# Kernel optimization log

Measured on AMD Instinct MI355X. Metric: run time of the kernel, lower is better.

Reference implementation:

```python
import jax, jax.numpy as jnp
import numpy as np

B, S, NX, NH = 4, 1024, 1024, 16
HD = NX // NH  # head_features = 64


def setup_inputs() -> dict:
    key = jax.random.key(0)
    k1, k2, k3 = jax.random.split(key, 3)
    x = jax.random.normal(k1, (B, S, NX), dtype=jnp.float32)
    w_attn = 0.02 * jax.random.normal(k2, (NX, 3 * NX), dtype=jnp.float32)
    b_attn = jnp.zeros((3 * NX,), dtype=jnp.float32)
    w_proj = 0.02 * jax.random.normal(k3, (NX, NX), dtype=jnp.float32)
    b_proj = jnp.zeros((NX,), dtype=jnp.float32)
    causal_bias = jnp.tril(jnp.ones((S, S), dtype=jnp.float32))  # tril buffer
    return {"x": x, "w_attn": w_attn, "b_attn": b_attn,
            "w_proj": w_proj, "b_proj": b_proj, "causal_bias": causal_bias}


def reference(x, w_attn, b_attn, w_proj, b_proj, causal_bias):
    # c_attn: fused qkv projection (Conv1D == addmm)
    qkv = x @ w_attn + b_attn                     # [B, S, 3*NX]
    q, k, v = jnp.split(qkv, 3, axis=-1)          # each [B, S, NX]
    # split heads -> [B, H, S, D]
    q = q.reshape(B, S, NH, HD).transpose(0, 2, 1, 3)
    k = k.reshape(B, S, NH, HD).transpose(0, 2, 1, 3)
    v = v.reshape(B, S, NH, HD).transpose(0, 2, 1, 3)
    # present: stack of (key in [B,H,S,D] layout, value)
    present = jnp.stack((k, v))                   # [2, B, H, S, D]
    # scores with scale=True
    w = jnp.einsum('bhqd,bhkd->bhqk', q, k) / jnp.sqrt(jnp.float32(HD))
    b = causal_bias[None, None, :, :]             # [1,1,S,S] (nd==ns==S)
    w = w * b - 1e10 * (1.0 - b)                  # multiplicative mask trick
    p = jax.nn.softmax(w, axis=-1)
    a = jnp.einsum('bhqk,bhkd->bhqd', p, v)       # [B, H, S, D]
    a = a.transpose(0, 2, 1, 3).reshape(B, S, NX)  # merge heads
    out = a @ w_proj + b_proj                     # c_proj
    return out, present
```

## Files before the change

kernel.cpp:

```cpp
#include <hip/hip_runtime.h>
#include <hip/hip_bf16.h>

typedef __attribute__((ext_vector_type(8))) short short8;
typedef __attribute__((ext_vector_type(4))) float floatx4;

constexpr int Bsz = 4, Ssz = 1024, NXc = 1024, NHc = 16, HDc = 64;
constexpr int OUT_ELEMS  = Bsz * Ssz * NXc;
constexpr int HEAD_ELEMS = Bsz * NHc * Ssz * HDc;

union BF8 { __hip_bfloat16 h[8]; uint4 v; short8 s; };

__device__ __forceinline__ uint4 cvt8(const float* __restrict__ p) {
    float4 a = *reinterpret_cast<const float4*>(p);
    float4 b = *reinterpret_cast<const float4*>(p + 4);
    BF8 u;
    u.h[0] = __float2bfloat16(a.x); u.h[1] = __float2bfloat16(a.y);
    u.h[2] = __float2bfloat16(a.z); u.h[3] = __float2bfloat16(a.w);
    u.h[4] = __float2bfloat16(b.x); u.h[5] = __float2bfloat16(b.y);
    u.h[6] = __float2bfloat16(b.z); u.h[7] = __float2bfloat16(b.w);
    return u.v;
}

__device__ __forceinline__ void load_lds_16B(const void* g, void* l) {
    __builtin_amdgcn_global_load_lds(
        (const __attribute__((address_space(1))) unsigned int*)g,
        (__attribute__((address_space(3))) unsigned int*)l, 16, 0, 0);
}


__global__ __launch_bounds__(256) void prep_kernel(
    const float* __restrict__ x, __hip_bfloat16* __restrict__ x_bf,
    const float* __restrict__ w_attn, __hip_bfloat16* __restrict__ wTa,
    const float* __restrict__ w_proj, __hip_bfloat16* __restrict__ wTp)
{
    const int bid = blockIdx.x, tid = threadIdx.x;
    __shared__ float t[64][65];
    if (bid < 2048) {
        const int i = (bid * 256 + tid) * 8;
        *reinterpret_cast<uint4*>(x_bf + i) = cvt8(x + i);
        return;
    }
    const float* in; __hip_bfloat16* outp; int N, bx, by;
    if (bid < 2816) { const int q = bid - 2048; in = w_attn; outp = wTa; N = 3072; bx = q % 48; by = q / 48; }
    else            { const int q = bid - 2816; in = w_proj; outp = wTp; N = 1024; bx = q % 16; by = q / 16; }
    const int k0 = by * 64, n0 = bx * 64;
#pragma unroll
    for (int j = 0; j < 16; ++j) {
        const int idx = tid + j * 256;
        const int row = idx >> 6, col = idx & 63;
        t[row][col] = in[(size_t)(k0 + row) * N + n0 + col];
    }
    __syncthreads();
#pragma unroll
    for (int j = 0; j < 16; ++j) {
        const int idx = tid + j * 256;
        const int orow = idx >> 6, ocol = idx & 63;
        outp[(size_t)(n0 + orow) * 1024 + k0 + ocol] = __float2bfloat16(t[ocol][orow]);
    }
}

template <int EPI>
__global__ __launch_bounds__(256) void gemm128p(
    const __hip_bfloat16* __restrict__ A,
    const __hip_bfloat16* __restrict__ Bt,
    const float* __restrict__ bias,
    float* __restrict__ outf,
    __hip_bfloat16* __restrict__ qws,
    float* __restrict__ present,
    __hip_bfloat16* __restrict__ kws,
    __hip_bfloat16* __restrict__ vtws,
    int M, int N, int K)
{
    __shared__ __align__(16) __hip_bfloat16 As[3][4096];
    __shared__ __align__(16) __hip_bfloat16 Bs[3][4096];

    const int nbx = N >> 7;
    const int nwg = (M >> 7) * nbx;
    const int wg  = blockIdx.x;
    const int swz = (wg & 7) * (nwg >> 3) + (wg >> 3);
    const int by  = swz / nbx, bx = swz % nbx;

    const int tid  = threadIdx.x;
    const int w    = tid >> 6, lane = tid & 63;
    const int quad = lane >> 4, l16 = lane & 15;
    const int m0 = by * 128, n0 = bx * 128;
    const int mb = (w >> 1) * 64, nbw = (w & 1) * 64;

    const int srow = lane >> 2;
    const int sksw = (((lane & 3) ^ ((lane >> 3) & 3))) * 8;
    const int rsw = (l16 >> 1) & 3;

    floatx4 acc[4][4];
#pragma unroll
    for (int i = 0; i < 4; ++i)
#pragma unroll
        for (int j = 0; j < 4; ++j)
#pragma unroll
            for (int r = 0; r < 4; ++r) acc[i][j][r] = 0.f;

    auto stage = [&](int buf, int k0) {
#pragma unroll
        for (int c = 0; c < 2; ++c) {
            const int chunk = w * 2 + c;
            const int row = chunk * 16 + srow;
            load_lds_16B(A + (size_t)(m0 + row) * K + k0 + sksw,
                         &As[buf][chunk * 512]);
            load_lds_16B(Bt + (size_t)(n0 + row) * K + k0 + sksw,
                         &Bs[buf][chunk * 512]);
        }
    };

    stage(0, 0);
    int cb = 0;
    for (int k0 = 0; k0 < K; k0 += 32) {
        if (k0 + 32 < K) {
            const int nb_ = (cb == 2) ? 0 : cb + 1;
            stage(nb_, k0 + 32);
            asm volatile("s_waitcnt vmcnt(4)" ::: "memory");
        } else {
            asm volatile("s_waitcnt vmcnt(0)" ::: "memory");
        }
        __builtin_amdgcn_s_barrier();
        __builtin_amdgcn_sched_barrier(0);

        short8 af[4], bfr[4];
#pragma unroll
        for (int mi = 0; mi < 4; ++mi)
            af[mi] = *reinterpret_cast<const short8*>(
                &As[cb][(mb + mi * 16 + l16) * 32 + ((quad ^ rsw) * 8)]);
#pragma unroll
        for (int ni = 0; ni < 4; ++ni)
            bfr[ni] = *reinterpret_cast<const short8*>(
                &Bs[cb][(nbw + ni * 16 + l16) * 32 + ((quad ^ rsw) * 8)]);
        __builtin_amdgcn_s_setprio(1);
#pragma unroll
        for (int mi = 0; mi < 4; ++mi)
#pragma unroll
            for (int ni = 0; ni < 4; ++ni)
                acc[mi][ni] = __builtin_amdgcn_mfma_f32_16x16x32_bf16(
                    af[mi], bfr[ni], acc[mi][ni], 0, 0, 0);
        __builtin_amdgcn_s_setprio(0);

        cb = (cb == 2) ? 0 : cb + 1;
    }

#pragma unroll
    for (int mi = 0; mi < 4; ++mi) {
#pragma unroll
        for (int ni = 0; ni < 4; ++ni) {
            const int col = n0 + nbw + ni * 16 + l16;
            const float bsv = bias[col];
#pragma unroll
            for (int r = 0; r < 4; ++r) {
                const int row = m0 + mb + mi * 16 + quad * 4 + r;
                const float v = acc[mi][ni][r] + bsv;
                if (EPI == 0) {
                    const int seg = col >> 10;
                    const int c = col & 1023;
                    if (seg == 0) {
                        qws[(size_t)row * 1024 + c] = __float2bfloat16(v);
                    } else {
                        const int bq = row >> 10, s = row & 1023;
                        const int hh = c >> 6, d = c & 63;
                        const size_t idx =
                            ((size_t)((bq * 16 + hh) * 1024 + s)) * 64 + d;
                        const int kt = s >> 6, key = s & 63;
                        const size_t tbase =
                            ((size_t)((bq * 16 + hh) * 16 + kt)) * 4096;
                        if (seg == 1) {
                            present[idx] = v;
                            kws[tbase + key * 64 +
                                ((((d >> 3) ^ (key & 7)) << 3) | (d & 7))] =
                                __float2bfloat16(v);
                        } else {
                            present[HEAD_ELEMS + idx] = v;
                            vtws[tbase + d * 64 +
                                ((((key >> 3) ^ (d & 7)) << 3) | (key & 7))] =
                                __float2bfloat16(v);
                        }
                    }
                } else {
                    outf[(size_t)row * N + col] = v;
                }
            }
        }
    }
}

__global__ __launch_bounds__(256) void attn_v5(
    const __hip_bfloat16* __restrict__ q_ws,
    const __hip_bfloat16* __restrict__ k_ws,
    const __hip_bfloat16* __restrict__ vt_ws,
    __hip_bfloat16* __restrict__ a_ws)
{
    const int wg  = blockIdx.x;
    const int swz = (wg & 7) * 128 + (wg >> 3);
    const int qt  = 15 - (swz & 15);
    const int bh  = swz >> 4;
    const int b = bh >> 4, h = bh & 15;

    const int tid  = threadIdx.x;
    const int wave = tid >> 6, lane = tid & 63;
    const int quad = lane >> 4, l16 = lane & 15;
    const int stripe = wave * 16;

    const __hip_bfloat16* Kbase = k_ws  + (size_t)bh * 65536;
    const __hip_bfloat16* Vbase = vt_ws + (size_t)bh * 65536;

    __shared__ __align__(16) __hip_bfloat16 Ksf[2][4096];
    __shared__ __align__(16) __hip_bfloat16 Vsf[2][4096];
    __shared__ __align__(16) __hip_bfloat16 Ps[64][72];

    constexpr float SCL = 0.18033688011f;

    const __hip_bfloat16* Qb =
        q_ws + ((size_t)(b * Ssz + qt * 64 + stripe + l16)) * NXc + h * 64;
    const short8 qf0 = *reinterpret_cast<const short8*>(Qb + quad * 8);
    const short8 qf1 = *reinterpret_cast<const short8*>(Qb + 32 + quad * 8);

    float m_i[4], l_i[4];
#pragma unroll
    for (int r = 0; r < 4; ++r) { m_i[r] = -1e9f; l_i[r] = 0.f; }
    floatx4 oacc[4];
#pragma unroll
    for (int ni = 0; ni < 4; ++ni)
#pragma unroll
        for (int r = 0; r < 4; ++r) oacc[ni][r] = 0.f;

#pragma unroll
    for (int c2 = 0; c2 < 2; ++c2) {
        const int c = wave + c2 * 4;
        load_lds_16B(Kbase + c * 512 + (lane << 3), &Ksf[0][c * 512]);
        load_lds_16B(Vbase + c * 512 + (lane << 3), &Vsf[0][c * 512]);
    }

    int cw = 0;
    for (int kt = 0; kt <= qt; ++kt) {
        asm volatile("s_waitcnt vmcnt(0)" ::: "memory");
        __builtin_amdgcn_s_barrier();
        __builtin_amdgcn_sched_barrier(0);

        if (kt < qt) {
            const __hip_bfloat16* Kt = Kbase + (size_t)(kt + 1) * 4096;
            const __hip_bfloat16* Vt = Vbase + (size_t)(kt + 1) * 4096;
            const int nb_ = cw ^ 1;
#pragma unroll
            for (int c2 = 0; c2 < 2; ++c2) {
                const int c = wave + c2 * 4;
                load_lds_16B(Kt + c * 512 + (lane << 3), &Ksf[nb_][c * 512]);
                load_lds_16B(Vt + c * 512 + (lane << 3), &Vsf[nb_][c * 512]);
            }
        }

        floatx4 sacc[4];
#pragma unroll
        for (int ni = 0; ni < 4; ++ni)
#pragma unroll
            for (int r = 0; r < 4; ++r) sacc[ni][r] = 0.f;
        __builtin_amdgcn_s_setprio(1);
#pragma unroll
        for (int ni = 0; ni < 4; ++ni) {
            const int key = ni * 16 + l16;
            const int sw = key & 7;
            const short8 kf0 = *reinterpret_cast<const short8*>(
                &Ksf[cw][key * 64 + ((quad ^ sw) << 3)]);
            const short8 kf1 = *reinterpret_cast<const short8*>(
                &Ksf[cw][key * 64 + (((4 + quad) ^ sw) << 3)]);
            sacc[ni] = __builtin_amdgcn_mfma_f32_16x16x32_bf16(
                qf0, kf0, sacc[ni], 0, 0, 0);
            sacc[ni] = __builtin_amdgcn_mfma_f32_16x16x32_bf16(
                qf1, kf1, sacc[ni], 0, 0, 0);
        }
        __builtin_amdgcn_s_setprio(0);

        const bool diag = (kt == qt);
        float alpha_[4];
#pragma unroll
        for (int r = 0; r < 4; ++r) {
            const int lrow = stripe + quad * 4 + r;
            float sv[4];
            float mx = -1e30f;
#pragma unroll
            for (int ni = 0; ni < 4; ++ni) {
                float v = sacc[ni][r] * SCL;
                if (diag && (ni * 16 + l16) > lrow) v = -1e9f;
                sv[ni] = v;
                mx = fmaxf(mx, v);
            }
            mx = fmaxf(mx, __shfl_xor(mx, 1));
            mx = fmaxf(mx, __shfl_xor(mx, 2));
            mx = fmaxf(mx, __shfl_xor(mx, 4));
            mx = fmaxf(mx, __shfl_xor(mx, 8));
            const float mnew = fmaxf(m_i[r], mx);
            const float al = exp2f(m_i[r] - mnew);
            m_i[r] = mnew;
            float s = 0.f;
#pragma unroll
            for (int nn = 0; nn < 4; ++nn) {
                const int ni = (nn + quad) & 3;
                const float p = exp2f(sv[ni] - mnew);
                s += p;
                Ps[lrow][ni * 16 + l16] = __float2bfloat16(p);
            }
            s += __shfl_xor(s, 1);
            s += __shfl_xor(s, 2);
            s += __shfl_xor(s, 4);
            s += __shfl_xor(s, 8);
            l_i[r] = l_i[r] * al + s;
            alpha_[r] = al;
        }

#pragma unroll
        for (int ni = 0; ni < 4; ++ni)
#pragma unroll
            for (int r = 0; r < 4; ++r) oacc[ni][r] *= alpha_[r];

        __builtin_amdgcn_s_setprio(1);
#pragma unroll
        for (int kk = 0; kk < 64; kk += 32) {
            const short8 pf = *reinterpret_cast<const short8*>(
                &Ps[stripe + l16][kk + quad * 8]);
#pragma unroll
            for (int ni = 0; ni < 4; ++ni) {
                const int d = ni * 16 + l16;
                const int chunk = (kk >> 3) + quad;
                const short8 vf = *reinterpret_cast<const short8*>(
                    &Vsf[cw][d * 64 + ((chunk ^ (d & 7)) << 3)]);
                oacc[ni] = __builtin_amdgcn_mfma_f32_16x16x32_bf16(
                    pf, vf, oacc[ni], 0, 0, 0);
            }
        }
        __builtin_amdgcn_s_setprio(0);

        cw ^= 1;
    }

#pragma unroll
    for (int ni = 0; ni < 4; ++ni) {
#pragma unroll
        for (int r = 0; r < 4; ++r) {
            const int row = qt * 64 + stripe + quad * 4 + r;
            const int col = h * 64 + ni * 16 + l16;
            const float inv = 1.0f / fmaxf(l_i[r], 1e-20f);
            a_ws[((size_t)(b * Ssz + row)) * NXc + col] =
                __float2bfloat16(oacc[ni][r] * inv);
        }
    }
}

template <int EPI>
__global__ __launch_bounds__(256) void gemm64(
    const void* __restrict__ Av, const float* __restrict__ Bw,
    const float* __restrict__ bias, float* __restrict__ out0,
    float* __restrict__ present, int M, int N, int K)
{
    __shared__ __align__(16) __hip_bfloat16 As[64][40];
    __shared__ __align__(16) __hip_bfloat16 Bs[64][40];
    const int tid = threadIdx.x;
    const int wave = tid >> 6, lane = tid & 63;
    const int quad = lane >> 4, l16 = lane & 15;
    const int m0 = blockIdx.y * 64, n0 = blockIdx.x * 64;
    const int mb = (wave >> 1) * 32, nb = (wave & 1) * 32;
    const int arow = tid >> 2, aseg = tid & 3;
    const int brow = tid >> 3, bseg = tid & 7;
    floatx4 acc[2][2];
#pragma unroll
    for (int i = 0; i < 2; ++i)
#pragma unroll
        for (int j = 0; j < 2; ++j)
#pragma unroll
            for (int r = 0; r < 4; ++r) acc[i][j][r] = 0.f;
    for (int k0 = 0; k0 < K; k0 += 32) {
        if (EPI == 0) {
            const float* A = (const float*)Av;
            *reinterpret_cast<uint4*>(&As[arow][aseg * 8]) =
                cvt8(A + (size_t)(m0 + arow) * K + k0 + aseg * 8);
        } else {
            const __hip_bfloat16* A = (const __hip_bfloat16*)Av;
            *reinterpret_cast<uint4*>(&As[arow][aseg * 8]) =
                *reinterpret_cast<const uint4*>(
                    A + (size_t)(m0 + arow) * K + k0 + aseg * 8);
        }
        const float* bp = Bw + (size_t)(k0 + brow) * N + n0 + bseg * 8;
        float4 b0 = *reinterpret_cast<const float4*>(bp);
        float4 b1 = *reinterpret_cast<const float4*>(bp + 4);
        Bs[bseg * 8 + 0][brow] = __float2bfloat16(b0.x);
        Bs[bseg * 8 + 1][brow] = __float2bfloat16(b0.y);
        Bs[bseg * 8 + 2][brow] = __float2bfloat16(b0.z);
        Bs[bseg * 8 + 3][brow] = __float2bfloat16(b0.w);
        Bs[bseg * 8 + 4][brow] = __float2bfloat16(b1.x);
        Bs[bseg * 8 + 5][brow] = __float2bfloat16(b1.y);
        Bs[bseg * 8 + 6][brow] = __float2bfloat16(b1.z);
        Bs[bseg * 8 + 7][brow] = __float2bfloat16(b1.w);
        __syncthreads();
        short8 af[2], bf[2];
#pragma unroll
        for (int mm = 0; mm < 2; ++mm)
            af[mm] = *reinterpret_cast<const short8*>(&As[mb + mm * 16 + l16][quad * 8]);
#pragma unroll
        for (int nn = 0; nn < 2; ++nn)
            bf[nn] = *reinterpret_cast<const short8*>(&Bs[nb + nn * 16 + l16][quad * 8]);
#pragma unroll
        for (int mm = 0; mm < 2; ++mm)
#pragma unroll
            for (int nn = 0; nn < 2; ++nn)
                acc[mm][nn] = __builtin_amdgcn_mfma_f32_16x16x32_bf16(
                    af[mm], bf[nn], acc[mm][nn], 0, 0, 0);
        __syncthreads();
    }
#pragma unroll
    for (int mm = 0; mm < 2; ++mm)
#pragma unroll
        for (int nn = 0; nn < 2; ++nn) {
            const int col = n0 + nb + nn * 16 + l16;
            const float bsv = bias[col];
#pragma unroll
            for (int r = 0; r < 4; ++r) {
                const int row = m0 + mb + mm * 16 + quad * 4 + r;
                const float v = acc[mm][nn][r] + bsv;
                if (EPI == 0) {
                    const int seg = col >> 10;
                    const int c = col & 1023;
                    if (seg == 0) out0[(size_t)row * 1024 + c] = v;
                    else {
                        const int b = row >> 10, s = row & 1023;
                        const int h = c >> 6, d = c & 63;
                        const size_t idx = ((size_t)((b * 16 + h) * 1024 + s)) * 64 + d;
                        if (seg == 1) present[idx] = v;
                        else          present[HEAD_ELEMS + idx] = v;
                    }
                } else out0[(size_t)row * N + col] = v;
            }
        }
}

__global__ __launch_bounds__(256) void attn64(
    const float* __restrict__ qbuf, const float* __restrict__ present,
    __hip_bfloat16* __restrict__ a_ws)
{
    const int qt = blockIdx.x, h = blockIdx.y, b = blockIdx.z;
    const int tid = threadIdx.x;
    const int wave = tid >> 6, lane = tid & 63;
    const int quad = lane >> 4, l16 = lane & 15;
    const int mb = (wave >> 1) * 32, nb = (wave & 1) * 32;
    const size_t headoff = ((size_t)(b * 16 + h)) * Ssz * HDc;
    const float* Qb = qbuf + ((size_t)(b * Ssz + qt * 64)) * NXc + h * 64;
    const float* Kp = present + headoff;
    const float* Vp = present + HEAD_ELEMS + headoff;
    __shared__ __align__(16) __hip_bfloat16 Qs[64][72];
    __shared__ __align__(16) __hip_bfloat16 Ks[64][72];
    __shared__ __align__(16) __hip_bfloat16 Vts[64][72];
    __shared__ __align__(16) __hip_bfloat16 Ps[64][72];
    __shared__ float Sc[64][65];
    __shared__ float mrow[64], lrow[64], arw[64];
#pragma unroll
    for (int it = 0; it < 2; ++it) {
        const int c = tid + it * 256;
        const int row = c >> 3, seg = c & 7;
        *reinterpret_cast<uint4*>(&Qs[row][seg * 8]) =
            cvt8(Qb + (size_t)row * NXc + seg * 8);
    }
    if (tid < 64) { mrow[tid] = -1e9f; lrow[tid] = 0.f; }
    floatx4 oacc[2][2];
#pragma unroll
    for (int i = 0; i < 2; ++i)
#pragma unroll
        for (int j = 0; j < 2; ++j)
#pragma unroll
            for (int r = 0; r < 4; ++r) oacc[i][j][r] = 0.f;
    __syncthreads();
    for (int kt = 0; kt <= qt; ++kt) {
#pragma unroll
        for (int it = 0; it < 2; ++it) {
            const int c = tid + it * 256;
            const int row = c >> 3, seg = c & 7;
            *reinterpret_cast<uint4*>(&Ks[row][seg * 8]) =
                cvt8(Kp + (size_t)(kt * 64 + row) * 64 + seg * 8);
            const float* vp = Vp + (size_t)(kt * 64 + row) * 64 + seg * 8;
            float4 v0 = *reinterpret_cast<const float4*>(vp);
            float4 v1 = *reinterpret_cast<const float4*>(vp + 4);
            Vts[seg * 8 + 0][row] = __float2bfloat16(v0.x);
            Vts[seg * 8 + 1][row] = __float2bfloat16(v0.y);
            Vts[seg * 8 + 2][row] = __float2bfloat16(v0.z);
            Vts[seg * 8 + 3][row] = __float2bfloat16(v0.w);
            Vts[seg * 8 + 4][row] = __float2bfloat16(v1.x);
            Vts[seg * 8 + 5][row] = __float2bfloat16(v1.y);
            Vts[seg * 8 + 6][row] = __float2bfloat16(v1.z);
            Vts[seg * 8 + 7][row] = __float2bfloat16(v1.w);
        }
        __syncthreads();
        floatx4 sacc[2][2];
#pragma unroll
        for (int i = 0; i < 2; ++i)
#pragma unroll
            for (int j = 0; j < 2; ++j)
#pragma unroll
                for (int r = 0; r < 4; ++r) sacc[i][j][r] = 0.f;
#pragma unroll
        for (int kd = 0; kd < 64; kd += 32) {
            short8 af[2], bf[2];
#pragma unroll
            for (int mm = 0; mm < 2; ++mm)
                af[mm] = *reinterpret_cast<const short8*>(&Qs[mb + mm * 16 + l16][kd + quad * 8]);
#pragma unroll
            for (int nn = 0; nn < 2; ++nn)
                bf[nn] = *reinterpret_cast<const short8*>(&Ks[nb + nn * 16 + l16][kd + quad * 8]);
#pragma unroll
            for (int mm = 0; mm < 2; ++mm)
#pragma unroll
                for (int nn = 0; nn < 2; ++nn)
                    sacc[mm][nn] = __builtin_amdgcn_mfma_f32_16x16x32_bf16(
                        af[mm], bf[nn], sacc[mm][nn], 0, 0, 0);
        }
        const bool diag = (kt == qt);
#pragma unroll
        for (int mm = 0; mm < 2; ++mm)
#pragma unroll
            for (int nn = 0; nn < 2; ++nn)
#pragma unroll
                for (int r = 0; r < 4; ++r) {
                    const int row = mb + mm * 16 + quad * 4 + r;
                    const int col = nb + nn * 16 + l16;
                    float v = fminf(fmaxf(sacc[mm][nn][r] * 0.125f, -1e8f), 1e8f);
                    if (diag && col > row) v = -1e9f;
                    Sc[row][col] = v;
                }
        __syncthreads();
        if (tid < 64) {
            const int r = tid;
            const float mo = mrow[r];
            float mx = mo;
            for (int c = 0; c < 64; ++c) mx = fmaxf(mx, Sc[r][c]);
            const float al = (mo <= -5e8f) ? 0.f : __expf(mo - mx);
            float sum = 0.f;
            for (int c = 0; c < 64; ++c) {
                const float sv = Sc[r][c];
                const float p = (sv <= -5e8f) ? 0.f : __expf(sv - mx);
                sum += p;
                Ps[r][c] = __float2bfloat16(p);
            }
            mrow[r] = mx;
            lrow[r] = lrow[r] * al + sum;
            arw[r]  = al;
        }
        __syncthreads();
#pragma unroll
        for (int mm = 0; mm < 2; ++mm) {
            const int rbase = mb + mm * 16 + quad * 4;
#pragma unroll
            for (int r = 0; r < 4; ++r) {
                const float al = arw[rbase + r];
                oacc[mm][0][r] *= al;
                oacc[mm][1][r] *= al;
            }
        }
#pragma unroll
        for (int kk = 0; kk < 64; kk += 32) {
            short8 pf[2], vf[2];
#pragma unroll
            for (int mm = 0; mm < 2; ++mm)
                pf[mm] = *reinterpret_cast<const short8*>(&Ps[mb + mm * 16 + l16][kk + quad * 8]);
#pragma unroll
            for (int nn = 0; nn < 2; ++nn)
                vf[nn] = *reinterpret_cast<const short8*>(&Vts[nb + nn * 16 + l16][kk + quad * 8]);
#pragma unroll
            for (int mm = 0; mm < 2; ++mm)
#pragma unroll
                for (int nn = 0; nn < 2; ++nn)
                    oacc[mm][nn] = __builtin_amdgcn_mfma_f32_16x16x32_bf16(
                        pf[mm], vf[nn], oacc[mm][nn], 0, 0, 0);
        }
        __syncthreads();
    }
#pragma unroll
    for (int mm = 0; mm < 2; ++mm)
#pragma unroll
        for (int nn = 0; nn < 2; ++nn)
#pragma unroll
            for (int r = 0; r < 4; ++r) {
                const int row = mb + mm * 16 + quad * 4 + r;
                const int col = nb + nn * 16 + l16;
                const float inv = 1.0f / fmaxf(lrow[row], 1e-20f);
                a_ws[((size_t)(b * Ssz + qt * 64 + row)) * NXc + h * 64 + col] =
                    __float2bfloat16(oacc[mm][nn][r] * inv);
            }
}

extern "C" void kernel_launch(void* const* d_in, const int* in_sizes, int n_in,
                              void* d_out, int out_size, void* d_ws, size_t ws_size,
                              hipStream_t stream) {
    const float* x      = (const float*)d_in[0];
    const float* w_attn = (const float*)d_in[1];
    const float* b_attn = (const float*)d_in[2];
    const float* w_proj = (const float*)d_in[3];
    const float* b_proj = (const float*)d_in[4];

    float* out     = (float*)d_out;
    float* present = out + OUT_ELEMS;

    const size_t NEED = 32u * 1024u * 1024u;
    if (ws_size >= NEED) {
        __hip_bfloat16* reg1 = (__hip_bfloat16*)d_ws;
        __hip_bfloat16* reg2 = reg1 + 4194304;
        __hip_bfloat16* reg3 = reg2 + 4194304;
        __hip_bfloat16* wTa  = reg3 + 4194304;
        __hip_bfloat16* wTp  = wTa + 3145728;
        __hip_bfloat16* kws  = (__hip_bfloat16*)out;
        __hip_bfloat16* vtws = kws + 4194304;

        prep_kernel<<<3072, 256, 0, stream>>>(x, reg1, w_attn, wTa, w_proj, wTp);

        gemm128p<0><<<768, 256, 0, stream>>>(
            reg1, wTa, b_attn, nullptr, reg2, present, kws, vtws,
            4096, 3072, 1024);

        attn_v5<<<1024, 256, 0, stream>>>(reg2, kws, vtws, reg2);

        gemm128p<1><<<256, 256, 0, stream>>>(
            reg2, wTp, b_proj, out, nullptr, nullptr, nullptr, nullptr,
            4096, 1024, 1024);
    } else {
        __hip_bfloat16* a_ws = (__hip_bfloat16*)d_ws;
        hipMemsetAsync(d_ws, 0, (size_t)OUT_ELEMS * sizeof(__hip_bfloat16), stream);
        gemm64<0><<<dim3(48, 64), 256, 0, stream>>>(x, w_attn, b_attn, out, present,
                                                    4096, 3072, 1024);
        attn64<<<dim3(16, 16, 4), 256, 0, stream>>>(out, present, a_ws);
        gemm64<1><<<dim3(16, 64), 256, 0, stream>>>(a_ws, w_proj, b_proj, out, nullptr,
                                                    4096, 1024, 1024);
    }
}
```

Before: 213.7 us.

## Pair causal query tiles per block and deepen K/V prefetch to four buffers

```diff
diff --git a/kernel.cpp b/kernel.cpp
--- a/kernel.cpp
+++ b/kernel.cpp
@@ -187,16 +187,16 @@
     }
 }
 
-__global__ __launch_bounds__(256) void attn_v5(
+__global__ __launch_bounds__(256) void attn_v6(
     const __hip_bfloat16* __restrict__ q_ws,
     const __hip_bfloat16* __restrict__ k_ws,
     const __hip_bfloat16* __restrict__ vt_ws,
     __hip_bfloat16* __restrict__ a_ws)
 {
     const int wg  = blockIdx.x;
-    const int swz = (wg & 7) * 128 + (wg >> 3);
-    const int qt  = 15 - (swz & 15);
-    const int bh  = swz >> 4;
+    const int swz = (wg & 7) * 64 + (wg >> 3);
+    const int bx  = swz & 7;
+    const int bh  = swz >> 3;
     const int b = bh >> 4, h = bh & 15;
 
     const int tid  = threadIdx.x;
@@ -207,143 +207,161 @@
     const __hip_bfloat16* Kbase = k_ws  + (size_t)bh * 65536;
     const __hip_bfloat16* Vbase = vt_ws + (size_t)bh * 65536;
 
-    __shared__ __align__(16) __hip_bfloat16 Ksf[2][4096];
-    __shared__ __align__(16) __hip_bfloat16 Vsf[2][4096];
+    __shared__ __align__(16) __hip_bfloat16 Ksf[4][4096];
+    __shared__ __align__(16) __hip_bfloat16 Vsf[4][4096];
     __shared__ __align__(16) __hip_bfloat16 Ps[64][72];
 
     constexpr float SCL = 0.18033688011f;
 
-    const __hip_bfloat16* Qb =
-        q_ws + ((size_t)(b * Ssz + qt * 64 + stripe + l16)) * NXc + h * 64;
-    const short8 qf0 = *reinterpret_cast<const short8*>(Qb + quad * 8);
-    const short8 qf1 = *reinterpret_cast<const short8*>(Qb + 32 + quad * 8);
-
-    float m_i[4], l_i[4];
-#pragma unroll
-    for (int r = 0; r < 4; ++r) { m_i[r] = -1e9f; l_i[r] = 0.f; }
-    floatx4 oacc[4];
-#pragma unroll
-    for (int ni = 0; ni < 4; ++ni)
-#pragma unroll
-        for (int r = 0; r < 4; ++r) oacc[ni][r] = 0.f;
-
-#pragma unroll
-    for (int c2 = 0; c2 < 2; ++c2) {
-        const int c = wave + c2 * 4;
-        load_lds_16B(Kbase + c * 512 + (lane << 3), &Ksf[0][c * 512]);
-        load_lds_16B(Vbase + c * 512 + (lane << 3), &Vsf[0][c * 512]);
-    }
-
-    int cw = 0;
-    for (int kt = 0; kt <= qt; ++kt) {
-        asm volatile("s_waitcnt vmcnt(0)" ::: "memory");
-        __builtin_amdgcn_s_barrier();
-        __builtin_amdgcn_sched_barrier(0);
-
-        if (kt < qt) {
-            const __hip_bfloat16* Kt = Kbase + (size_t)(kt + 1) * 4096;
-            const __hip_bfloat16* Vt = Vbase + (size_t)(kt + 1) * 4096;
-            const int nb_ = cw ^ 1;
+#pragma unroll
+    for (int pass = 0; pass < 2; ++pass) {
+        const int qt = (pass == 0) ? (8 + bx) : (7 - bx);
+
+        const __hip_bfloat16* Qb =
+            q_ws + ((size_t)(b * Ssz + qt * 64 + stripe + l16)) * NXc + h * 64;
+        const short8 qf0 = *reinterpret_cast<const short8*>(Qb + quad * 8);
+        const short8 qf1 = *reinterpret_cast<const short8*>(Qb + 32 + quad * 8);
+
+        float m_i[4], l_i[4];
+#pragma unroll
+        for (int r = 0; r < 4; ++r) { m_i[r] = -1e9f; l_i[r] = 0.f; }
+        floatx4 oacc[4];
+#pragma unroll
+        for (int ni = 0; ni < 4; ++ni)
+#pragma unroll
+            for (int r = 0; r < 4; ++r) oacc[ni][r] = 0.f;
+
+#pragma unroll
+        for (int c2 = 0; c2 < 2; ++c2) {
+            const int c = wave + c2 * 4;
+            load_lds_16B(Kbase + c * 512 + (lane << 3), &Ksf[0][c * 512]);
+            load_lds_16B(Vbase + c * 512 + (lane << 3), &Vsf[0][c * 512]);
+        }
+        if (qt >= 1) {
 #pragma unroll
             for (int c2 = 0; c2 < 2; ++c2) {
                 const int c = wave + c2 * 4;
-                load_lds_16B(Kt + c * 512 + (lane << 3), &Ksf[nb_][c * 512]);
-                load_lds_16B(Vt + c * 512 + (lane << 3), &Vsf[nb_][c * 512]);
-            }
-        }
-
-        floatx4 sacc[4];
-#pragma unroll
-        for (int ni = 0; ni < 4; ++ni)
-#pragma unroll
-            for (int r = 0; r < 4; ++r) sacc[ni][r] = 0.f;
-        __builtin_amdgcn_s_setprio(1);
+                load_lds_16B(Kbase + 4096 + c * 512 + (lane << 3),
+                             &Ksf[1][c * 512]);
+                load_lds_16B(Vbase + 4096 + c * 512 + (lane << 3),
+                             &Vsf[1][c * 512]);
+            }
+        }
+
+        for (int kt = 0; kt <= qt; ++kt) {
+            const int cw = kt & 3;
+            if (kt + 2 <= qt) {
+                const int nb_ = (kt + 2) & 3;
+                const __hip_bfloat16* Kt = Kbase + (size_t)(kt + 2) * 4096;
+                const __hip_bfloat16* Vt = Vbase + (size_t)(kt + 2) * 4096;
+#pragma unroll
+                for (int c2 = 0; c2 < 2; ++c2) {
+                    const int c = wave + c2 * 4;
+                    load_lds_16B(Kt + c * 512 + (lane << 3), &Ksf[nb_][c * 512]);
+                    load_lds_16B(Vt + c * 512 + (lane << 3), &Vsf[nb_][c * 512]);
+                }
+                asm volatile("s_waitcnt vmcnt(8)" ::: "memory");
+            } else if (kt + 1 <= qt) {
+                asm volatile("s_waitcnt vmcnt(4)" ::: "memory");
+            } else {
+                asm volatile("s_waitcnt vmcnt(0)" ::: "memory");
+            }
+            __builtin_amdgcn_s_barrier();
+            __builtin_amdgcn_sched_barrier(0);
+
+            floatx4 sacc[4];
+#pragma unroll
+            for (int ni = 0; ni < 4; ++ni)
+#pragma unroll
+                for (int r = 0; r < 4; ++r) sacc[ni][r] = 0.f;
+            __builtin_amdgcn_s_setprio(1);
+#pragma unroll
+            for (int ni = 0; ni < 4; ++ni) {
+                const int key = ni * 16 + l16;
+                const int sw = key & 7;
+                const short8 kf0 = *reinterpret_cast<const short8*>(
+                    &Ksf[cw][key * 64 + ((quad ^ sw) << 3)]);
+                const short8 kf1 = *reinterpret_cast<const short8*>(
+                    &Ksf[cw][key * 64 + (((4 + quad) ^ sw) << 3)]);
+                sacc[ni] = __builtin_amdgcn_mfma_f32_16x16x32_bf16(
+                    qf0, kf0, sacc[ni], 0, 0, 0);
+                sacc[ni] = __builtin_amdgcn_mfma_f32_16x16x32_bf16(
+                    qf1, kf1, sacc[ni], 0, 0, 0);
+            }
+            __builtin_amdgcn_s_setprio(0);
+
+            const bool diag = (kt == qt);
+            float alpha_[4];
+#pragma unroll
+            for (int r = 0; r < 4; ++r) {
+                const int lrow = stripe + quad * 4 + r;
+                float sv[4];
+                float mx = -1e30f;
+#pragma unroll
+                for (int ni = 0; ni < 4; ++ni) {
+                    float v = sacc[ni][r] * SCL;
+                    if (diag && (ni * 16 + l16) > lrow) v = -1e9f;
+                    sv[ni] = v;
+                    mx = fmaxf(mx, v);
+                }
+                mx = fmaxf(mx, __shfl_xor(mx, 1));
+                mx = fmaxf(mx, __shfl_xor(mx, 2));
+                mx = fmaxf(mx, __shfl_xor(mx, 4));
+                mx = fmaxf(mx, __shfl_xor(mx, 8));
+                const float mnew = fmaxf(m_i[r], mx);
+                const float al = exp2f(m_i[r] - mnew);
+                m_i[r] = mnew;
+                float s = 0.f;
+#pragma unroll
+                for (int nn = 0; nn < 4; ++nn) {
+                    const int ni = (nn + quad) & 3;
+                    const float p = exp2f(sv[ni] - mnew);
+                    s += p;
+                    Ps[lrow][ni * 16 + l16] = __float2bfloat16(p);
+                }
+                s += __shfl_xor(s, 1);
+                s += __shfl_xor(s, 2);
+                s += __shfl_xor(s, 4);
+                s += __shfl_xor(s, 8);
+                l_i[r] = l_i[r] * al + s;
+                alpha_[r] = al;
+            }
+
+#pragma unroll
+            for (int ni = 0; ni < 4; ++ni)
+#pragma unroll
+                for (int r = 0; r < 4; ++r) oacc[ni][r] *= alpha_[r];
+
+            __builtin_amdgcn_s_setprio(1);
+#pragma unroll
+            for (int kk = 0; kk < 64; kk += 32) {
+                const short8 pf = *reinterpret_cast<const short8*>(
+                    &Ps[stripe + l16][kk + quad * 8]);
+#pragma unroll
+                for (int ni = 0; ni < 4; ++ni) {
+                    const int d = ni * 16 + l16;
+                    const int chunk = (kk >> 3) + quad;
+                    const short8 vf = *reinterpret_cast<const short8*>(
+                        &Vsf[cw][d * 64 + ((chunk ^ (d & 7)) << 3)]);
+                    oacc[ni] = __builtin_amdgcn_mfma_f32_16x16x32_bf16(
+                        pf, vf, oacc[ni], 0, 0, 0);
+                }
+            }
+            __builtin_amdgcn_s_setprio(0);
+        }
+
+        __builtin_amdgcn_s_barrier();
+
 #pragma unroll
         for (int ni = 0; ni < 4; ++ni) {
-            const int key = ni * 16 + l16;
-            const int sw = key & 7;
-            const short8 kf0 = *reinterpret_cast<const short8*>(
-                &Ksf[cw][key * 64 + ((quad ^ sw) << 3)]);
-            const short8 kf1 = *reinterpret_cast<const short8*>(
-                &Ksf[cw][key * 64 + (((4 + quad) ^ sw) << 3)]);
-            sacc[ni] = __builtin_amdgcn_mfma_f32_16x16x32_bf16(
-                qf0, kf0, sacc[ni], 0, 0, 0);
-            sacc[ni] = __builtin_amdgcn_mfma_f32_16x16x32_bf16(
-                qf1, kf1, sacc[ni], 0, 0, 0);
-        }
-        __builtin_amdgcn_s_setprio(0);
-
-        const bool diag = (kt == qt);
-        float alpha_[4];
-#pragma unroll
-        for (int r = 0; r < 4; ++r) {
-            const int lrow = stripe + quad * 4 + r;
-            float sv[4];
-            float mx = -1e30f;
-#pragma unroll
-            for (int ni = 0; ni < 4; ++ni) {
-                float v = sacc[ni][r] * SCL;
-                if (diag && (ni * 16 + l16) > lrow) v = -1e9f;
-                sv[ni] = v;
-                mx = fmaxf(mx, v);
-            }
-            mx = fmaxf(mx, __shfl_xor(mx, 1));
-            mx = fmaxf(mx, __shfl_xor(mx, 2));
-            mx = fmaxf(mx, __shfl_xor(mx, 4));
-            mx = fmaxf(mx, __shfl_xor(mx, 8));
-            const float mnew = fmaxf(m_i[r], mx);
-            const float al = exp2f(m_i[r] - mnew);
-            m_i[r] = mnew;
-            float s = 0.f;
-#pragma unroll
-            for (int nn = 0; nn < 4; ++nn) {
-                const int ni = (nn + quad) & 3;
-                const float p = exp2f(sv[ni] - mnew);
-                s += p;
-                Ps[lrow][ni * 16 + l16] = __float2bfloat16(p);
-            }
-            s += __shfl_xor(s, 1);
-            s += __shfl_xor(s, 2);
-            s += __shfl_xor(s, 4);
-            s += __shfl_xor(s, 8);
-            l_i[r] = l_i[r] * al + s;
-            alpha_[r] = al;
-        }
-
-#pragma unroll
-        for (int ni = 0; ni < 4; ++ni)
-#pragma unroll
-            for (int r = 0; r < 4; ++r) oacc[ni][r] *= alpha_[r];
-
-        __builtin_amdgcn_s_setprio(1);
-#pragma unroll
-        for (int kk = 0; kk < 64; kk += 32) {
-            const short8 pf = *reinterpret_cast<const short8*>(
-                &Ps[stripe + l16][kk + quad * 8]);
-#pragma unroll
-            for (int ni = 0; ni < 4; ++ni) {
-                const int d = ni * 16 + l16;
-                const int chunk = (kk >> 3) + quad;
-                const short8 vf = *reinterpret_cast<const short8*>(
-                    &Vsf[cw][d * 64 + ((chunk ^ (d & 7)) << 3)]);
-                oacc[ni] = __builtin_amdgcn_mfma_f32_16x16x32_bf16(
-                    pf, vf, oacc[ni], 0, 0, 0);
-            }
-        }
-        __builtin_amdgcn_s_setprio(0);
-
-        cw ^= 1;
-    }
-
-#pragma unroll
-    for (int ni = 0; ni < 4; ++ni) {
-#pragma unroll
-        for (int r = 0; r < 4; ++r) {
-            const int row = qt * 64 + stripe + quad * 4 + r;
-            const int col = h * 64 + ni * 16 + l16;
-            const float inv = 1.0f / fmaxf(l_i[r], 1e-20f);
-            a_ws[((size_t)(b * Ssz + row)) * NXc + col] =
-                __float2bfloat16(oacc[ni][r] * inv);
+#pragma unroll
+            for (int r = 0; r < 4; ++r) {
+                const int row = qt * 64 + stripe + quad * 4 + r;
+                const int col = h * 64 + ni * 16 + l16;
+                const float inv = 1.0f / fmaxf(l_i[r], 1e-20f);
+                a_ws[((size_t)(b * Ssz + row)) * NXc + col] =
+                    __float2bfloat16(oacc[ni][r] * inv);
+            }
         }
     }
 }
@@ -614,7 +632,7 @@
             reg1, wTa, b_attn, nullptr, reg2, present, kws, vtws,
             4096, 3072, 1024);
 
-        attn_v5<<<1024, 256, 0, stream>>>(reg2, kws, vtws, reg2);
+        attn_v6<<<512, 256, 0, stream>>>(reg2, kws, vtws, reg2);
 
         gemm128p<1><<<256, 256, 0, stream>>>(
             reg2, wTp, b_proj, out, nullptr, nullptr, nullptr, nullptr,
```

After: 197.4 us. 7.7% less time.
